# Optimization experiments

Measured on AMD Instinct MI355X. Metric: run time of the kernel, lower is better.

## Reference

```python
import jax, jax.numpy as jnp
import numpy as np

D_MODEL = 1024
NUM_HEADS = 16
D_K = D_MODEL // NUM_HEADS
ROPE_THETA = 10000.0


def apply_rope(x, theta=ROPE_THETA):
    # x: [B, H, S, d_k]; rotate interleaved even/odd pairs by pos*theta^(-2i/d)
    S, d = x.shape[-2], x.shape[-1]
    pos = jnp.arange(S, dtype=x.dtype)
    inv_freq = theta ** (-jnp.arange(0, d, 2, dtype=x.dtype) / d)  # [d/2]
    ang = pos[:, None] * inv_freq[None, :]  # [S, d/2]
    cos, sin = jnp.cos(ang), jnp.sin(ang)
    x1, x2 = x[..., 0::2], x[..., 1::2]
    o1 = x1 * cos - x2 * sin
    o2 = x1 * sin + x2 * cos
    return jnp.stack([o1, o2], axis=-1).reshape(x.shape)


def setup_inputs() -> dict:
    key = jax.random.key(0)
    ks = jax.random.split(key, 5)
    B, S, D = 2, 2048, D_MODEL
    x = jax.random.normal(ks[0], (B, S, D), dtype=jnp.float32)
    scale = 0.02
    W_q = jax.random.normal(ks[1], (D, D), dtype=jnp.float32) * scale
    W_k = jax.random.normal(ks[2], (D, D), dtype=jnp.float32) * scale
    W_v = jax.random.normal(ks[3], (D, D), dtype=jnp.float32) * scale
    W_o = jax.random.normal(ks[4], (D, D), dtype=jnp.float32) * scale
    return {"x": x, "W_q": W_q, "W_k": W_k, "W_v": W_v, "W_o": W_o}


def reference(x, W_q, W_k, W_v, W_o):
    B, S, D = x.shape
    H, dk = NUM_HEADS, D_K
    # projections (Linear: y = x @ W.T, no bias)
    q = (x @ W_q.T).reshape(B, S, H, dk).transpose(0, 2, 1, 3)  # [B,H,S,dk]
    k = (x @ W_k.T).reshape(B, S, H, dk).transpose(0, 2, 1, 3)
    v = (x @ W_v.T).reshape(B, S, H, dk).transpose(0, 2, 1, 3)
    q = apply_rope(q)
    k = apply_rope(k)
    scores = jnp.einsum('bhqd,bhkd->bhqk', q, k) / jnp.sqrt(jnp.asarray(dk, x.dtype))
    causal = jnp.tril(jnp.ones((S, S), dtype=bool))
    scores = jnp.where(causal, scores, jnp.asarray(-jnp.inf, x.dtype))
    probs = jax.nn.softmax(scores, axis=-1)
    attn = jnp.einsum('bhqk,bhkd->bhqd', probs, v)  # [B,H,S,dk]
    attn = attn.transpose(0, 2, 1, 3).reshape(B, S, D)
    return attn @ W_o.T
```

## Files before the change

### kernel.cpp

```cpp
#include <hip/hip_runtime.h>

#define D_MODEL 1024
#define NHEAD 16
#define DK 64
#define SEQ 2048
#define NBATCH 2
#define MROWS (NBATCH * SEQ)

typedef unsigned short u16;
typedef short bf16x8 __attribute__((ext_vector_type(8)));
typedef float f32x4 __attribute__((ext_vector_type(4)));
typedef unsigned short u16x8 __attribute__((ext_vector_type(8)));

__device__ __forceinline__ u16 f2bf(float f) {
    union { float f; unsigned u; } v; v.f = f;
    unsigned r = v.u + 0x7FFFu + ((v.u >> 16) & 1u);
    return (u16)(r >> 16);
}

__device__ __forceinline__ void gload16(const void* g, void* s) {
    __builtin_amdgcn_global_load_lds((const __attribute__((address_space(1))) void*)g,
                                     (__attribute__((address_space(3))) void*)s, 16, 0, 0);
}

#define XN 4194304
#define WN 1048576

__global__ __launch_bounds__(256) void convert_bf16(
    const float* __restrict__ x, const float* __restrict__ wq, const float* __restrict__ wk,
    const float* __restrict__ wv, const float* __restrict__ wo,
    u16* __restrict__ xb, u16* __restrict__ wqkv, u16* __restrict__ wob)
{
    size_t base = ((size_t)blockIdx.x * 256 + threadIdx.x) * 8;
    const float* src; u16* dst;
    if (base < XN)               { src = x  + base;                dst = xb   + base; }
    else if (base < XN + WN)     { src = wq + (base - XN);         dst = wqkv + (base - XN); }
    else if (base < XN + 2*WN)   { src = wk + (base - XN - WN);    dst = wqkv + (base - XN); }
    else if (base < XN + 3*WN)   { src = wv + (base - XN - 2*WN);  dst = wqkv + (base - XN); }
    else                         { src = wo + (base - XN - 3*WN);  dst = wob  + (base - XN - 3*WN); }
    float4 a = *(const float4*)&src[0];
    float4 b = *(const float4*)&src[4];
    u16x8 o;
    o[0] = f2bf(a.x); o[1] = f2bf(a.y); o[2] = f2bf(a.z); o[3] = f2bf(a.w);
    o[4] = f2bf(b.x); o[5] = f2bf(b.y); o[6] = f2bf(b.z); o[7] = f2bf(b.w);
    *(u16x8*)dst = o;
}

__global__ __launch_bounds__(256) void fill_rope(float* __restrict__ rc, float* __restrict__ rs)
{
    int idx = blockIdx.x * 256 + threadIdx.x;
    int d2 = idx >> 11, s = idx & 2047;
    const float lnth = 9.210340371976184f;
    float invf = __expf(-lnth * (float)(2 * d2) * (1.0f / 64.0f));
    float sn, cs;
    __sincosf((float)s * invf, &sn, &cs);
    rc[idx] = cs;
    rs[idx] = sn;
}

__global__ __launch_bounds__(256) void gemm_qkv(
    const u16* __restrict__ A, const u16* __restrict__ B,
    const float* __restrict__ ropec, const float* __restrict__ ropes,
    u16* __restrict__ qo, u16* __restrict__ ko, u16* __restrict__ vo)
{
    __shared__ __align__(16) u16 sbuf[17408];

    const int tid = threadIdx.x, w = tid >> 6, l = tid & 63;
    const int l15 = l & 15, lg = l >> 4;
    const int m0 = blockIdx.x * 128, n0 = blockIdx.y * 128;
    const int wm = (w >> 1) * 64, wn = (w & 1) * 64;

    f32x4 zero = {0.f, 0.f, 0.f, 0.f};
    f32x4 acc[4][4];
#pragma unroll
    for (int i = 0; i < 4; ++i)
#pragma unroll
        for (int j = 0; j < 4; ++j) acc[i][j] = zero;

    auto stage = [&](int k0s, int half) {
        const int hb = half * 8192;
#pragma unroll
        for (int it = 0; it < 2; ++it) {
            int ubase = it * 256 + w * 64;
            int u = ubase + l, row = u >> 2, kq = u & 3;
            gload16(A + (size_t)(m0 + row) * D_MODEL + k0s + kq * 8, &sbuf[hb + ubase * 8]);
        }
#pragma unroll
        for (int it = 0; it < 2; ++it) {
            int ubase = it * 256 + w * 64;
            int u = ubase + l, row = u >> 2, kq = u & 3;
            gload16(B + (size_t)(n0 + row) * D_MODEL + k0s + kq * 8, &sbuf[hb + 4096 + ubase * 8]);
        }
    };

    stage(0, 0);
    int cur = 0;
    for (int k0 = 0; k0 < D_MODEL; k0 += 32, cur ^= 1) {
        __syncthreads();
        if (k0 + 32 < D_MODEL) stage(k0 + 32, cur ^ 1);
        const int hb = cur * 8192;
        bf16x8 af[4], bf[4];
#pragma unroll
        for (int mi = 0; mi < 4; ++mi) af[mi] = *(const bf16x8*)&sbuf[hb + (wm + mi * 16 + l15) * 32 + lg * 8];
#pragma unroll
        for (int ni = 0; ni < 4; ++ni) bf[ni] = *(const bf16x8*)&sbuf[hb + 4096 + (wn + ni * 16 + l15) * 32 + lg * 8];
#pragma unroll
        for (int mi = 0; mi < 4; ++mi)
#pragma unroll
            for (int ni = 0; ni < 4; ++ni)
                acc[mi][ni] = __builtin_amdgcn_mfma_f32_16x16x32_bf16(af[mi], bf[ni], acc[mi][ni], 0, 0, 0);
    }

    const int which = n0 >> 10;
    if (which < 2) {
        u16* outp = (which == 0) ? qo : ko;
        const float qscale = 0.125f * 1.44269504088896340736f;
#pragma unroll
        for (int ni = 0; ni < 4; ++ni) {
            int n = n0 + wn + ni * 16 + l15;
            int hh = (n >> 6) & 15, d = n & 63;
            const float* rcb = ropec + (d >> 1) * 2048;
            const float* rsb = ropes + (d >> 1) * 2048;
            float sgn = (d & 1) ? 1.0f : -1.0f;
#pragma unroll
            for (int mi = 0; mi < 4; ++mi) {
                int mbase = m0 + wm + mi * 16 + lg * 4;
                int bb = mbase >> 11, sb = mbase & (SEQ - 1);
                float4 c4 = *(const float4*)&rcb[sb];
                float4 s4v = *(const float4*)&rsb[sb];
                float cr[4] = {c4.x, c4.y, c4.z, c4.w};
                float sr[4] = {s4v.x, s4v.y, s4v.z, s4v.w};
#pragma unroll
                for (int i = 0; i < 4; ++i) {
                    float v = acc[mi][ni][i];
                    float pv = __shfl_xor(v, 1);
                    float res = v * cr[i] + sgn * pv * sr[i];
                    if (which == 0) res *= qscale;
                    outp[((size_t)(bb * NHEAD + hh) * SEQ + sb + i) * DK + d] = f2bf(res);
                }
            }
        }
    } else {
        __syncthreads();
        u16* sc = &sbuf[w * 64 * 68];
#pragma unroll
        for (int mi = 0; mi < 4; ++mi)
#pragma unroll
            for (int ni = 0; ni < 4; ++ni)
#pragma unroll
                for (int i = 0; i < 4; ++i)
                    sc[(mi * 16 + lg * 4 + i) * 68 + ni * 16 + l15] = f2bf(acc[mi][ni][i]);
        int vcol = n0 - 2048 + wn;
        int hh = vcol >> 6;
        int m = m0 + wm, bb = m >> 11, s0 = m & (SEQ - 1);
        u16* dst = vo + ((size_t)(bb * NHEAD + hh) * DK + l) * SEQ + s0;
#pragma unroll
        for (int j8 = 0; j8 < 8; ++j8) {
            u16x8 val;
#pragma unroll
            for (int jj = 0; jj < 8; ++jj) val[jj] = sc[(j8 * 8 + jj) * 68 + l];
            *(u16x8*)&dst[j8 * 8] = val;
        }
    }
}

__global__ __launch_bounds__(256, 4) void attn_mfma(
    const u16* __restrict__ qb, const u16* __restrict__ kb,
    const u16* __restrict__ vtb, u16* __restrict__ attnb)
{
    __shared__ __align__(16) u16 Kt[2][4096];
    __shared__ __align__(16) u16 Vt[2][4096];
    __shared__ __align__(16) u16 Ps_all[4096];

    const int id = blockIdx.x;
    const int bh = id & 31;
    const int g = (id >> 5) & 7, r = id >> 8;
    const int qt = (r == 0) ? g : (r == 1) ? (15 - g) : (r == 2) ? (16 + g) : (31 - g);
    const int b = bh >> 4, h = bh & 15;
    const int qbase = qt * 64;
    const int tid = threadIdx.x, w = tid >> 6, l = tid & 63;
    const int l15 = l & 15, lg = l >> 4;

    const u16* qlane = qb + ((size_t)bh * SEQ + qbase + w * 16 + l15) * DK + lg * 8;
    bf16x8 bq[2];
    bq[0] = *(const bf16x8*)&qlane[0];
    bq[1] = *(const bf16x8*)&qlane[32];

    const u16* kg = kb + (size_t)bh * SEQ * DK;
    const u16* vg = vtb + (size_t)bh * DK * SEQ;

    f32x4 zero = {0.f, 0.f, 0.f, 0.f};
    f32x4 ot[4];
#pragma unroll
    for (int i = 0; i < 4; ++i) ot[i] = zero;
    float mrun = -1e30f, lrun = 0.f;
    const int qg = qbase + w * 16 + l15;

    char* Psb = (char*)&Ps_all[w * 1024];
    const int swz = (l15 & 7) << 4;

    auto stageKV = [&](int kt2, int half) {
        const int kc2 = kt2 * 64;
#pragma unroll
        for (int it = 0; it < 2; ++it) {
            int ubase = it * 256 + w * 64;
            int u = ubase + l, rr = u >> 3, cq = u & 7;
            gload16(kg + (size_t)(kc2 + rr) * DK + ((cq ^ (rr & 7)) << 3), &Kt[half][ubase * 8]);
            gload16(vg + (size_t)rr * SEQ + kc2 + ((cq ^ (rr & 7)) << 3), &Vt[half][ubase * 8]);
        }
    };

    stageKV(0, 0);
    int cur = 0;
    for (int kt = 0; kt <= qt; ++kt, cur ^= 1) {
        const int kc = kt * 64;
        __syncthreads();
        if (kt < qt) stageKV(kt + 1, cur ^ 1);

        f32x4 s4[4];
        __builtin_amdgcn_s_setprio(1);
#pragma unroll
        for (int ni = 0; ni < 4; ++ni) {
            s4[ni] = zero;
#pragma unroll
            for (int kk = 0; kk < 2; ++kk) {
                int row = ni * 16 + l15, cq2 = kk * 4 + lg;
                bf16x8 kf = *(const bf16x8*)&Kt[cur][(row * 8 + (cq2 ^ (row & 7))) * 8];
                s4[ni] = __builtin_amdgcn_mfma_f32_16x16x32_bf16(kf, bq[kk], s4[ni], 0, 0, 0);
            }
        }
        __builtin_amdgcn_s_setprio(0);
        if (kt == qt) {
#pragma unroll
            for (int ni = 0; ni < 4; ++ni)
#pragma unroll
                for (int i = 0; i < 4; ++i)
                    if (kc + ni * 16 + lg * 4 + i > qg) s4[ni][i] = -1e30f;
        }

        float mx = -1e30f;
#pragma unroll
        for (int ni = 0; ni < 4; ++ni)
            mx = fmaxf(mx, fmaxf(fmaxf(s4[ni][0], s4[ni][1]), fmaxf(s4[ni][2], s4[ni][3])));
        mx = fmaxf(mx, __shfl_xor(mx, 16));
        mx = fmaxf(mx, __shfl_xor(mx, 32));
        if (!__all(mx - mrun <= 8.0f)) {
            float mn2 = fmaxf(mrun, mx);
            float scl = __builtin_amdgcn_exp2f(mrun - mn2);
            mrun = mn2;
            lrun *= scl;
#pragma unroll
            for (int n2 = 0; n2 < 4; ++n2)
#pragma unroll
                for (int i = 0; i < 4; ++i) ot[n2][i] *= scl;
        }
        float rs = 0.f;
#pragma unroll
        for (int ni = 0; ni < 4; ++ni)
#pragma unroll
            for (int ih = 0; ih < 2; ++ih) {
                float p0 = __builtin_amdgcn_exp2f(s4[ni][2 * ih] - mrun);
                float p1 = __builtin_amdgcn_exp2f(s4[ni][2 * ih + 1] - mrun);
                rs += p0 + p1;
                unsigned pw = (unsigned)f2bf(p0) | ((unsigned)f2bf(p1) << 16);
                int bytecol = ni * 32 + lg * 8 + ih * 4;
                *(unsigned*)(Psb + (l15 << 7) + (bytecol ^ swz)) = pw;
            }
        rs += __shfl_xor(rs, 16);
        rs += __shfl_xor(rs, 32);
        lrun += rs;

        bf16x8 bp[2];
#pragma unroll
        for (int kk = 0; kk < 2; ++kk)
            bp[kk] = *(const bf16x8*)(Psb + (l15 << 7) + ((kk * 64 + lg * 16) ^ swz));

        __builtin_amdgcn_s_setprio(1);
#pragma unroll
        for (int n2 = 0; n2 < 4; ++n2)
#pragma unroll
            for (int kk = 0; kk < 2; ++kk) {
                int row = n2 * 16 + l15, cq2 = kk * 4 + lg;
                bf16x8 vf = *(const bf16x8*)&Vt[cur][(row * 8 + (cq2 ^ (row & 7))) * 8];
                ot[n2] = __builtin_amdgcn_mfma_f32_16x16x32_bf16(vf, bp[kk], ot[n2], 0, 0, 0);
            }
        __builtin_amdgcn_s_setprio(0);
    }

    const float invl = 1.0f / lrun;
    u16* orow = attnb + ((size_t)b * SEQ + qg) * D_MODEL + h * DK;
#pragma unroll
    for (int n2 = 0; n2 < 4; ++n2)
#pragma unroll
        for (int ih = 0; ih < 2; ++ih) {
            float r0 = ot[n2][2 * ih] * invl;
            float r1 = ot[n2][2 * ih + 1] * invl;
            unsigned pw = (unsigned)f2bf(r0) | ((unsigned)f2bf(r1) << 16);
            *(unsigned*)&orow[n2 * 16 + lg * 4 + 2 * ih] = pw;
        }
}

__global__ __launch_bounds__(256) void gemm_proj(
    const u16* __restrict__ A, const u16* __restrict__ B, float* __restrict__ out)
{
    __shared__ __align__(16) u16 sbuf[16384];

    const int tid = threadIdx.x, w = tid >> 6, l = tid & 63;
    const int l15 = l & 15, lg = l >> 4;
    const int m0 = blockIdx.x * 128, n0 = blockIdx.y * 128;
    const int wm = (w >> 1) * 64, wn = (w & 1) * 64;

    f32x4 zero = {0.f, 0.f, 0.f, 0.f};
    f32x4 acc[4][4];
#pragma unroll
    for (int i = 0; i < 4; ++i)
#pragma unroll
        for (int j = 0; j < 4; ++j) acc[i][j] = zero;

    auto stage = [&](int k0s, int half) {
        const int hb = half * 8192;
#pragma unroll
        for (int it = 0; it < 2; ++it) {
            int ubase = it * 256 + w * 64;
            int u = ubase + l, row = u >> 2, kq = u & 3;
            gload16(A + (size_t)(m0 + row) * D_MODEL + k0s + kq * 8, &sbuf[hb + ubase * 8]);
        }
#pragma unroll
        for (int it = 0; it < 2; ++it) {
            int ubase = it * 256 + w * 64;
            int u = ubase + l, row = u >> 2, kq = u & 3;
            gload16(B + (size_t)(n0 + row) * D_MODEL + k0s + kq * 8, &sbuf[hb + 4096 + ubase * 8]);
        }
    };

    stage(0, 0);
    int cur = 0;
    for (int k0 = 0; k0 < D_MODEL; k0 += 32, cur ^= 1) {
        __syncthreads();
        if (k0 + 32 < D_MODEL) stage(k0 + 32, cur ^ 1);
        const int hb = cur * 8192;
        bf16x8 af[4], bf[4];
#pragma unroll
        for (int mi = 0; mi < 4; ++mi) af[mi] = *(const bf16x8*)&sbuf[hb + (wm + mi * 16 + l15) * 32 + lg * 8];
#pragma unroll
        for (int ni = 0; ni < 4; ++ni) bf[ni] = *(const bf16x8*)&sbuf[hb + 4096 + (wn + ni * 16 + l15) * 32 + lg * 8];
#pragma unroll
        for (int mi = 0; mi < 4; ++mi)
#pragma unroll
            for (int ni = 0; ni < 4; ++ni)
                acc[mi][ni] = __builtin_amdgcn_mfma_f32_16x16x32_bf16(af[mi], bf[ni], acc[mi][ni], 0, 0, 0);
    }

#pragma unroll
    for (int mi = 0; mi < 4; ++mi)
#pragma unroll
        for (int ni = 0; ni < 4; ++ni)
#pragma unroll
            for (int i = 0; i < 4; ++i) {
                int m = m0 + wm + mi * 16 + lg * 4 + i;
                int n = n0 + wn + ni * 16 + l15;
                out[(size_t)m * D_MODEL + n] = acc[mi][ni][i];
            }
}

extern "C" void kernel_launch(void* const* d_in, const int* in_sizes, int n_in,
                              void* d_out, int out_size, void* d_ws, size_t ws_size,
                              hipStream_t stream) {
    const float* x  = (const float*)d_in[0];
    const float* Wq = (const float*)d_in[1];
    const float* Wk = (const float*)d_in[2];
    const float* Wv = (const float*)d_in[3];
    const float* Wo = (const float*)d_in[4];
    float* out = (float*)d_out;

    u16* ws = (u16*)d_ws;
    const size_t M1 = 1048576;
    u16* xb    = ws;
    u16* wqkv  = ws + 4 * M1;
    u16* wob   = ws + 7 * M1;
    u16* qb    = ws + 8 * M1;
    u16* kb    = ws + 12 * M1;
    u16* vtb   = ws + 16 * M1;
    u16* attnb = ws + 20 * M1;
    float* ropec = (float*)(ws + 24 * M1);
    float* ropes = (float*)(ws + 24 * M1) + 65536;

    convert_bf16<<<dim3(4096), dim3(256), 0, stream>>>(x, Wq, Wk, Wv, Wo, xb, wqkv, wob);
    fill_rope<<<dim3(256), dim3(256), 0, stream>>>(ropec, ropes);
    gemm_qkv<<<dim3(MROWS / 128, 3072 / 128), dim3(256), 0, stream>>>(xb, wqkv, ropec, ropes, qb, kb, vtb);
    attn_mfma<<<dim3(1024), dim3(256), 0, stream>>>(qb, kb, vtb, attnb);
    gemm_proj<<<dim3(MROWS / 128, D_MODEL / 128), dim3(256), 0, stream>>>(attnb, wob, out);
}
```

Measured before the change: 186.8 us.

## Use 128-row query tiles with 512-thread attention blocks and fold rope fill into convert

The attention kernel now runs 8 waves per block over 128 query rows, so each staged K/V tile is shared by twice as many queries. Each thread stages one 16-byte chunk instead of two. Waves skip key tiles that lie entirely above their causal diagonal, and masking is applied only on tiles that cross it. Separately, the rope table fill is merged into the convert kernel as extra blocks, which removes one launch. Trade-offs: the grid is halved to 512 blocks, per-block work is more uneven across causal rows, and waves in a block idle at the barrier while others process diagonal tiles.

```diff
diff --git a/kernel.cpp b/kernel.cpp
--- a/kernel.cpp
+++ b/kernel.cpp
@@ -29,8 +29,20 @@
 __global__ __launch_bounds__(256) void convert_bf16(
     const float* __restrict__ x, const float* __restrict__ wq, const float* __restrict__ wk,
     const float* __restrict__ wv, const float* __restrict__ wo,
-    u16* __restrict__ xb, u16* __restrict__ wqkv, u16* __restrict__ wob)
+    u16* __restrict__ xb, u16* __restrict__ wqkv, u16* __restrict__ wob,
+    float* __restrict__ rc, float* __restrict__ rs)
 {
+    if (blockIdx.x >= 4096) {
+        int idx = (blockIdx.x - 4096) * 256 + threadIdx.x;
+        int d2 = idx >> 11, s = idx & 2047;
+        const float lnth = 9.210340371976184f;
+        float invf = __expf(-lnth * (float)(2 * d2) * (1.0f / 64.0f));
+        float sn, cs;
+        __sincosf((float)s * invf, &sn, &cs);
+        rc[idx] = cs;
+        rs[idx] = sn;
+        return;
+    }
     size_t base = ((size_t)blockIdx.x * 256 + threadIdx.x) * 8;
     const float* src; u16* dst;
     if (base < XN)               { src = x  + base;                dst = xb   + base; }
@@ -46,18 +58,6 @@
     *(u16x8*)dst = o;
 }
 
-__global__ __launch_bounds__(256) void fill_rope(float* __restrict__ rc, float* __restrict__ rs)
-{
-    int idx = blockIdx.x * 256 + threadIdx.x;
-    int d2 = idx >> 11, s = idx & 2047;
-    const float lnth = 9.210340371976184f;
-    float invf = __expf(-lnth * (float)(2 * d2) * (1.0f / 64.0f));
-    float sn, cs;
-    __sincosf((float)s * invf, &sn, &cs);
-    rc[idx] = cs;
-    rs[idx] = sn;
-}
-
 __global__ __launch_bounds__(256) void gemm_qkv(
     const u16* __restrict__ A, const u16* __restrict__ B,
     const float* __restrict__ ropec, const float* __restrict__ ropes,
@@ -164,24 +164,27 @@
     }
 }
 
-__global__ __launch_bounds__(256, 4) void attn_mfma(
+__global__ __launch_bounds__(512, 4) void attn_mfma(
     const u16* __restrict__ qb, const u16* __restrict__ kb,
     const u16* __restrict__ vtb, u16* __restrict__ attnb)
 {
     __shared__ __align__(16) u16 Kt[2][4096];
     __shared__ __align__(16) u16 Vt[2][4096];
-    __shared__ __align__(16) u16 Ps_all[4096];
+    __shared__ __align__(16) u16 Ps_all[8192];
 
     const int id = blockIdx.x;
     const int bh = id & 31;
     const int g = (id >> 5) & 7, r = id >> 8;
-    const int qt = (r == 0) ? g : (r == 1) ? (15 - g) : (r == 2) ? (16 + g) : (31 - g);
+    const int qt = (r == 0) ? g : (15 - g);
     const int b = bh >> 4, h = bh & 15;
-    const int qbase = qt * 64;
+    const int qbase = qt * 128;
     const int tid = threadIdx.x, w = tid >> 6, l = tid & 63;
     const int l15 = l & 15, lg = l >> 4;
-
-    const u16* qlane = qb + ((size_t)bh * SEQ + qbase + w * 16 + l15) * DK + lg * 8;
+    const int qg = qbase + w * 16 + l15;
+    const int wmin = qbase + w * 16, wmax = wmin + 15;
+    const int ktmax = 2 * qt + 1;
+
+    const u16* qlane = qb + ((size_t)bh * SEQ + qg) * DK + lg * 8;
     bf16x8 bq[2];
     bq[0] = *(const bf16x8*)&qlane[0];
     bq[1] = *(const bf16x8*)&qlane[32];
@@ -194,97 +197,94 @@
 #pragma unroll
     for (int i = 0; i < 4; ++i) ot[i] = zero;
     float mrun = -1e30f, lrun = 0.f;
-    const int qg = qbase + w * 16 + l15;
 
     char* Psb = (char*)&Ps_all[w * 1024];
     const int swz = (l15 & 7) << 4;
 
     auto stageKV = [&](int kt2, int half) {
         const int kc2 = kt2 * 64;
-#pragma unroll
-        for (int it = 0; it < 2; ++it) {
-            int ubase = it * 256 + w * 64;
-            int u = ubase + l, rr = u >> 3, cq = u & 7;
-            gload16(kg + (size_t)(kc2 + rr) * DK + ((cq ^ (rr & 7)) << 3), &Kt[half][ubase * 8]);
-            gload16(vg + (size_t)rr * SEQ + kc2 + ((cq ^ (rr & 7)) << 3), &Vt[half][ubase * 8]);
-        }
+        int rr = tid >> 3, cq = tid & 7;
+        gload16(kg + (size_t)(kc2 + rr) * DK + ((cq ^ (rr & 7)) << 3), &Kt[half][tid * 8]);
+        gload16(vg + (size_t)rr * SEQ + kc2 + ((cq ^ (rr & 7)) << 3), &Vt[half][tid * 8]);
     };
 
     stageKV(0, 0);
     int cur = 0;
-    for (int kt = 0; kt <= qt; ++kt, cur ^= 1) {
+    for (int kt = 0; kt <= ktmax; ++kt, cur ^= 1) {
         const int kc = kt * 64;
         __syncthreads();
-        if (kt < qt) stageKV(kt + 1, cur ^ 1);
-
-        f32x4 s4[4];
-        __builtin_amdgcn_s_setprio(1);
-#pragma unroll
-        for (int ni = 0; ni < 4; ++ni) {
-            s4[ni] = zero;
-#pragma unroll
-            for (int kk = 0; kk < 2; ++kk) {
-                int row = ni * 16 + l15, cq2 = kk * 4 + lg;
-                bf16x8 kf = *(const bf16x8*)&Kt[cur][(row * 8 + (cq2 ^ (row & 7))) * 8];
-                s4[ni] = __builtin_amdgcn_mfma_f32_16x16x32_bf16(kf, bq[kk], s4[ni], 0, 0, 0);
-            }
-        }
-        __builtin_amdgcn_s_setprio(0);
-        if (kt == qt) {
-#pragma unroll
-            for (int ni = 0; ni < 4; ++ni)
-#pragma unroll
-                for (int i = 0; i < 4; ++i)
-                    if (kc + ni * 16 + lg * 4 + i > qg) s4[ni][i] = -1e30f;
-        }
-
-        float mx = -1e30f;
-#pragma unroll
-        for (int ni = 0; ni < 4; ++ni)
-            mx = fmaxf(mx, fmaxf(fmaxf(s4[ni][0], s4[ni][1]), fmaxf(s4[ni][2], s4[ni][3])));
-        mx = fmaxf(mx, __shfl_xor(mx, 16));
-        mx = fmaxf(mx, __shfl_xor(mx, 32));
-        if (!__all(mx - mrun <= 8.0f)) {
-            float mn2 = fmaxf(mrun, mx);
-            float scl = __builtin_amdgcn_exp2f(mrun - mn2);
-            mrun = mn2;
-            lrun *= scl;
+        if (kt < ktmax) stageKV(kt + 1, cur ^ 1);
+
+        if (kc <= wmax) {
+            f32x4 s4[4];
+            __builtin_amdgcn_s_setprio(1);
+#pragma unroll
+            for (int ni = 0; ni < 4; ++ni) {
+                s4[ni] = zero;
+#pragma unroll
+                for (int kk = 0; kk < 2; ++kk) {
+                    int row = ni * 16 + l15, cq2 = kk * 4 + lg;
+                    bf16x8 kf = *(const bf16x8*)&Kt[cur][(row * 8 + (cq2 ^ (row & 7))) * 8];
+                    s4[ni] = __builtin_amdgcn_mfma_f32_16x16x32_bf16(kf, bq[kk], s4[ni], 0, 0, 0);
+                }
+            }
+            __builtin_amdgcn_s_setprio(0);
+            if (kc + 63 > wmin) {
+#pragma unroll
+                for (int ni = 0; ni < 4; ++ni)
+#pragma unroll
+                    for (int i = 0; i < 4; ++i)
+                        if (kc + ni * 16 + lg * 4 + i > qg) s4[ni][i] = -1e30f;
+            }
+
+            float mx = -1e30f;
+#pragma unroll
+            for (int ni = 0; ni < 4; ++ni)
+                mx = fmaxf(mx, fmaxf(fmaxf(s4[ni][0], s4[ni][1]), fmaxf(s4[ni][2], s4[ni][3])));
+            mx = fmaxf(mx, __shfl_xor(mx, 16));
+            mx = fmaxf(mx, __shfl_xor(mx, 32));
+            if (!__all(mx - mrun <= 8.0f)) {
+                float mn2 = fmaxf(mrun, mx);
+                float scl = __builtin_amdgcn_exp2f(mrun - mn2);
+                mrun = mn2;
+                lrun *= scl;
+#pragma unroll
+                for (int n2 = 0; n2 < 4; ++n2)
+#pragma unroll
+                    for (int i = 0; i < 4; ++i) ot[n2][i] *= scl;
+            }
+            float rs = 0.f;
+#pragma unroll
+            for (int ni = 0; ni < 4; ++ni)
+#pragma unroll
+                for (int ih = 0; ih < 2; ++ih) {
+                    float p0 = __builtin_amdgcn_exp2f(s4[ni][2 * ih] - mrun);
+                    float p1 = __builtin_amdgcn_exp2f(s4[ni][2 * ih + 1] - mrun);
+                    rs += p0 + p1;
+                    unsigned pw = (unsigned)f2bf(p0) | ((unsigned)f2bf(p1) << 16);
+                    int bytecol = ni * 32 + lg * 8 + ih * 4;
+                    *(unsigned*)(Psb + (l15 << 7) + (bytecol ^ swz)) = pw;
+                }
+            rs += __shfl_xor(rs, 16);
+            rs += __shfl_xor(rs, 32);
+            lrun += rs;
+
+            bf16x8 bp[2];
+#pragma unroll
+            for (int kk = 0; kk < 2; ++kk)
+                bp[kk] = *(const bf16x8*)(Psb + (l15 << 7) + ((kk * 64 + lg * 16) ^ swz));
+
+            __builtin_amdgcn_s_setprio(1);
 #pragma unroll
             for (int n2 = 0; n2 < 4; ++n2)
 #pragma unroll
-                for (int i = 0; i < 4; ++i) ot[n2][i] *= scl;
-        }
-        float rs = 0.f;
-#pragma unroll
-        for (int ni = 0; ni < 4; ++ni)
-#pragma unroll
-            for (int ih = 0; ih < 2; ++ih) {
-                float p0 = __builtin_amdgcn_exp2f(s4[ni][2 * ih] - mrun);
-                float p1 = __builtin_amdgcn_exp2f(s4[ni][2 * ih + 1] - mrun);
-                rs += p0 + p1;
-                unsigned pw = (unsigned)f2bf(p0) | ((unsigned)f2bf(p1) << 16);
-                int bytecol = ni * 32 + lg * 8 + ih * 4;
-                *(unsigned*)(Psb + (l15 << 7) + (bytecol ^ swz)) = pw;
-            }
-        rs += __shfl_xor(rs, 16);
-        rs += __shfl_xor(rs, 32);
-        lrun += rs;
-
-        bf16x8 bp[2];
-#pragma unroll
-        for (int kk = 0; kk < 2; ++kk)
-            bp[kk] = *(const bf16x8*)(Psb + (l15 << 7) + ((kk * 64 + lg * 16) ^ swz));
-
-        __builtin_amdgcn_s_setprio(1);
-#pragma unroll
-        for (int n2 = 0; n2 < 4; ++n2)
-#pragma unroll
-            for (int kk = 0; kk < 2; ++kk) {
-                int row = n2 * 16 + l15, cq2 = kk * 4 + lg;
-                bf16x8 vf = *(const bf16x8*)&Vt[cur][(row * 8 + (cq2 ^ (row & 7))) * 8];
-                ot[n2] = __builtin_amdgcn_mfma_f32_16x16x32_bf16(vf, bp[kk], ot[n2], 0, 0, 0);
-            }
-        __builtin_amdgcn_s_setprio(0);
+                for (int kk = 0; kk < 2; ++kk) {
+                    int row = n2 * 16 + l15, cq2 = kk * 4 + lg;
+                    bf16x8 vf = *(const bf16x8*)&Vt[cur][(row * 8 + (cq2 ^ (row & 7))) * 8];
+                    ot[n2] = __builtin_amdgcn_mfma_f32_16x16x32_bf16(vf, bp[kk], ot[n2], 0, 0, 0);
+                }
+            __builtin_amdgcn_s_setprio(0);
+        }
     }
 
     const float invl = 1.0f / lrun;
@@ -385,9 +385,8 @@
     float* ropec = (float*)(ws + 24 * M1);
     float* ropes = (float*)(ws + 24 * M1) + 65536;
 
-    convert_bf16<<<dim3(4096), dim3(256), 0, stream>>>(x, Wq, Wk, Wv, Wo, xb, wqkv, wob);
-    fill_rope<<<dim3(256), dim3(256), 0, stream>>>(ropec, ropes);
+    convert_bf16<<<dim3(4352), dim3(256), 0, stream>>>(x, Wq, Wk, Wv, Wo, xb, wqkv, wob, ropec, ropes);
     gemm_qkv<<<dim3(MROWS / 128, 3072 / 128), dim3(256), 0, stream>>>(xb, wqkv, ropec, ropes, qb, kb, vtb);
-    attn_mfma<<<dim3(1024), dim3(256), 0, stream>>>(qb, kb, vtb, attnb);
+    attn_mfma<<<dim3(512), dim3(512), 0, stream>>>(qb, kb, vtb, attnb);
     gemm_proj<<<dim3(MROWS / 128, D_MODEL / 128), dim3(256), 0, stream>>>(attnb, wob, out);
 }
```

Measured after the change: 187.7 us. No clear change (+0.5%).
